# Optimization experiments

Measured on AMD Instinct MI355X. Metric: run time of the kernel, lower is better.

Reference implementation:

```python
import jax, jax.numpy as jnp
import numpy as np

EPS = 1e-5
N, DEG, D, L = 50000, 16, 128, 2  # nodes, max_neighbor, embed_size, gnn_layer


def _log_map_zero(y):
    # Poincare ball log map at origin: atanh(||y||) * y / ||y||, with clamps
    n = jnp.linalg.norm(y, axis=-1, keepdims=True)
    nc = jnp.clip(n, EPS, 1.0 - EPS)
    return y * (jnp.arctanh(nc) / nc)


def _exp_map_zero(v):
    # Poincare ball exp map at origin: tanh(||v||) * v / ||v||
    n = jnp.linalg.norm(v, axis=-1, keepdims=True)
    nc = jnp.maximum(n, EPS)
    return v * (jnp.tanh(nc) / nc)


def setup_inputs() -> dict:
    key = jax.random.key(0)
    k1, k2, k3, k4, k5 = jax.random.split(key, 5)
    node_repr = jax.random.normal(k1, (N, D), jnp.float32) * 0.1
    adj = jax.random.randint(k2, (N, DEG), 0, N)
    weight = jax.random.normal(k3, (N, DEG), jnp.float32)
    mask = jnp.ones((N, 1), jnp.float32)
    # per-relation, per-layer message weights (2 relations: pos / neg edges)
    scale = 1.0 / np.sqrt(D)
    W_pos = jax.random.normal(k4, (L, D, D), jnp.float32) * scale
    W_neg = jax.random.normal(k5, (L, D, D), jnp.float32) * scale
    return {"node_repr": node_repr, "adj": adj, "weight": weight,
            "mask": mask, "W_pos": W_pos, "W_neg": W_neg}


def reference(node_repr, adj, weight, mask, W_pos, W_neg):
    # split_graph_by_negative_edge
    pos_m = (weight > 0).astype(weight.dtype)
    neg_m = (weight < 0).astype(weight.dtype)
    adjs = (adj * pos_m.astype(adj.dtype), adj * neg_m.astype(adj.dtype))
    ws = (weight * pos_m, (-weight) * neg_m)
    Ws = (W_pos, W_neg)

    x = node_repr
    for step in range(L):
        x = (_log_map_zero(x) if step > 0 else x) * mask
        combined = jnp.zeros_like(x)
        for a, w, W in zip(adjs, ws, Ws):
            msg = (x @ W[step]) * mask                    # [N, D]
            nb = msg[a.reshape(-1)].reshape(N, DEG, D)    # neighbor gather
            combined = combined + jnp.sum(w[..., None] * nb, axis=1)
        combined = combined * mask                        # dropout identity (eval)
        x = _exp_map_zero(combined) * mask
        x = jax.nn.relu(x) * mask                         # poincare activation
    return x
```

## Files before the change

### kernel.cpp

```cpp
#include <hip/hip_runtime.h>
#include <math.h>

#define DD 128
#define DEG 16
#define TM 16
#define LDST 136
#define EPSV 1e-5f

typedef _Float16 half8_t __attribute__((ext_vector_type(8)));
typedef float    f32x4   __attribute__((ext_vector_type(4)));
typedef signed char c16v __attribute__((ext_vector_type(16)));

__device__ __forceinline__ float fast_tanh_over(float n) {
    float e  = __expf(2.f * n);
    float th = 1.f - __fdividef(2.f, e + 1.f);
    return __fdividef(th, n);
}
__device__ __forceinline__ float fast_atanh_over(float n) {
    float r = 0.5f * __logf(__fdividef(1.f + n, 1.f - n));
    return __fdividef(r, n);
}

__global__ void prep(const float* __restrict__ x, const float* __restrict__ mask,
                     signed char* __restrict__ x8, float* __restrict__ xsc, int nA,
                     const float* __restrict__ Wp, const float* __restrict__ Wn,
                     _Float16* __restrict__ WT)
{
    if ((int)blockIdx.x < nA) {
        const int r   = blockIdx.x * 16 + (threadIdx.x >> 4);
        const int c16 = threadIdx.x & 15;
        float m  = mask[r];
        float m2 = m * m;
        const float4* xp = (const float4*)(x + (size_t)r * DD + c16 * 8);
        float4 a = xp[0], b = xp[1];
        float v[8] = {a.x*m2, a.y*m2, a.z*m2, a.w*m2, b.x*m2, b.y*m2, b.z*m2, b.w*m2};
        float mx = 0.f;
        #pragma unroll
        for (int c = 0; c < 8; ++c) mx = fmaxf(mx, fabsf(v[c]));
        mx = fmaxf(mx, __shfl_xor(mx, 1));
        mx = fmaxf(mx, __shfl_xor(mx, 2));
        mx = fmaxf(mx, __shfl_xor(mx, 4));
        mx = fmaxf(mx, __shfl_xor(mx, 8));
        float qs = __fdividef(127.f, fmaxf(mx, 1e-20f));
        int q[8];
        #pragma unroll
        for (int c = 0; c < 8; ++c) q[c] = __float2int_rn(v[c] * qs);
        unsigned lo = (q[0]&255) | ((q[1]&255)<<8) | ((q[2]&255)<<16) | ((unsigned)(q[3]&255)<<24);
        unsigned hi = (q[4]&255) | ((q[5]&255)<<8) | ((q[6]&255)<<16) | ((unsigned)(q[7]&255)<<24);
        *(uint2*)(x8 + (size_t)r * DD + c16 * 8) = make_uint2(lo, hi);
        if (c16 == 0) xsc[r] = mx * (1.f / 127.f);
    } else {
        int bid   = blockIdx.x - nA;
        int mat   = bid >> 3;
        int chunk = bid & 7;
        int l = mat >> 1, rel = mat & 1;
        const float* __restrict__ src = (rel ? Wn : Wp) + (size_t)l * DD * DD;
        _Float16* __restrict__ dst = WT + (size_t)mat * DD * DD;
        for (int o = chunk * 2048 + threadIdx.x; o < chunk * 2048 + 2048; o += 256) {
            int nn = o >> 7, kk = o & 127;
            dst[o] = (_Float16)src[kk * DD + nn];
        }
    }
}

__global__ __launch_bounds__(256, 2) void fused_layer(
    const signed char* __restrict__ src8,
    const float* __restrict__ sscale,
    const int*   __restrict__ adj, const float* __restrict__ wgt,
    const float* __restrict__ mask,
    const _Float16* __restrict__ WTp, const _Float16* __restrict__ WTn,
    float* __restrict__ dst_f32,
    signed char* __restrict__ dst8, float* __restrict__ dst_scale,
    int n, int apply_logmap)
{
    __shared__ __align__(16) _Float16 aggP[TM][LDST];
    __shared__ __align__(16) _Float16 aggN[TM][LDST];
    __shared__ int   eidxS[TM][DEG];
    __shared__ float ewgtS[TM][DEG];
    __shared__ float msh[TM];
    __shared__ float partA[4][TM];
    __shared__ float partB[4][TM];
    __shared__ float partC[4][TM];

    const int row0 = blockIdx.x * TM;
    const int tid  = threadIdx.x;

    {
        const int nd = tid >> 4, eg = tid & 15;
        int   av = adj[(size_t)(row0 + nd) * DEG + eg];
        float wv = wgt[(size_t)(row0 + nd) * DEG + eg];
        float sv = sscale[av];
        eidxS[nd][eg] = av;
        ewgtS[nd][eg] = wv * sv;
        if (tid < TM) msh[tid] = mask[row0 + tid];
    }
    __syncthreads();

    const int l64  = tid & 63;
    const int node = (tid >> 6) * 4 + (l64 >> 4);
    const int e    = (l64 >> 3) & 1;
    const int g    = l64 & 7;

    int   idxl[8];
    float wl[8];
    #pragma unroll
    for (int j = 0; j < 8; ++j) {
        idxl[j] = eidxS[node][2 * j + e];
        wl[j]   = ewgtS[node][2 * j + e];
    }

    float aP[16], aN[16];
    #pragma unroll
    for (int c = 0; c < 16; ++c) { aP[c] = 0.f; aN[c] = 0.f; }
    const signed char* __restrict__ srcg = src8 + g * 16;
    #pragma unroll
    for (int j = 0; j < 8; ++j) {
        c16v v = *(const c16v*)(srcg + ((size_t)idxl[j] << 7));
        float wp = fmaxf(wl[j], 0.f);
        float wn = fmaxf(-wl[j], 0.f);
        #pragma unroll
        for (int c = 0; c < 16; ++c) {
            float f = (float)v[c];
            aP[c] += wp * f;
            aN[c] += wn * f;
        }
    }
    {
        half8_t hP, hN;
        #pragma unroll
        for (int c = 0; c < 8; ++c) {
            float ownP  = e ? aP[8 + c] : aP[c];
            float sendP = e ? aP[c]     : aP[8 + c];
            float ownN  = e ? aN[8 + c] : aN[c];
            float sendN = e ? aN[c]     : aN[8 + c];
            hP[c] = (_Float16)(ownP + __shfl_xor(sendP, 8));
            hN[c] = (_Float16)(ownN + __shfl_xor(sendN, 8));
        }
        *(half8_t*)&aggP[node][g * 16 + e * 8] = hP;
        *(half8_t*)&aggN[node][g * 16 + e * 8] = hN;
    }
    __syncthreads();

    const int wv2  = tid >> 6;
    const int l15  = l64 & 15;
    const int quad = l64 >> 4;

    half8_t aPf[4], aNf[4];
    #pragma unroll
    for (int kb = 0; kb < 4; ++kb) {
        aPf[kb] = *(const half8_t*)&aggP[l15][kb * 32 + quad * 8];
        aNf[kb] = *(const half8_t*)&aggN[l15][kb * 32 + quad * 8];
    }

    f32x4 acc[2];
    acc[0] = (f32x4){0.f, 0.f, 0.f, 0.f};
    acc[1] = (f32x4){0.f, 0.f, 0.f, 0.f};
    #pragma unroll
    for (int t = 0; t < 2; ++t) {
        const int nb = wv2 * 2 + t;
        const _Float16* bp = WTp + (size_t)(nb * 16 + l15) * DD + quad * 8;
        const _Float16* bn = WTn + (size_t)(nb * 16 + l15) * DD + quad * 8;
        #pragma unroll
        for (int kb = 0; kb < 4; ++kb) {
            acc[t] = __builtin_amdgcn_mfma_f32_16x16x32_f16(
                aPf[kb], *(const half8_t*)(bp + kb * 32), acc[t], 0, 0, 0);
            acc[t] = __builtin_amdgcn_mfma_f32_16x16x32_f16(
                aNf[kb], *(const half8_t*)(bn + kb * 32), acc[t], 0, 0, 0);
        }
    }

    float cv0[4], cv1[4], mr[4];
    #pragma unroll
    for (int r = 0; r < 4; ++r) {
        const int rl  = quad * 4 + r;
        const int row = row0 + rl;
        float m = (row < n) ? msh[rl] : 0.f;
        mr[r] = m;
        float c0 = acc[0][r] * m, c1 = acc[1][r] * m;
        cv0[r] = c0; cv1[r] = c1;
        float p = c0 * c0 + c1 * c1;
        p += __shfl_xor(p, 1); p += __shfl_xor(p, 2);
        p += __shfl_xor(p, 4); p += __shfl_xor(p, 8);
        if (l15 == 0) partA[wv2][rl] = p;
    }
    __syncthreads();

    float x0[4], x1[4];
    #pragma unroll
    for (int r = 0; r < 4; ++r) {
        const int rl = quad * 4 + r;
        float c2 = partA[0][rl] + partA[1][rl] + partA[2][rl] + partA[3][rl];
        float nc = fmaxf(sqrtf(c2), EPSV);
        float sc = fast_tanh_over(nc);
        float m  = mr[r];
        float t0 = fmaxf(cv0[r] * sc * m, 0.f) * m;
        float t1 = fmaxf(cv1[r] * sc * m, 0.f) * m;
        x0[r] = t0; x1[r] = t1;
        if (apply_logmap) {
            float p = t0 * t0 + t1 * t1;
            p += __shfl_xor(p, 1); p += __shfl_xor(p, 2);
            p += __shfl_xor(p, 4); p += __shfl_xor(p, 8);
            if (l15 == 0) partB[wv2][rl] = p;
        }
    }

    if (apply_logmap) {
        __syncthreads();
        float y0r[4], y1r[4];
        #pragma unroll
        for (int r = 0; r < 4; ++r) {
            const int rl = quad * 4 + r;
            float s2  = partB[0][rl] + partB[1][rl] + partB[2][rl] + partB[3][rl];
            float nc2 = fminf(fmaxf(sqrtf(s2), EPSV), 1.f - EPSV);
            float f = fast_atanh_over(nc2) * mr[r] * mr[r];
            float y0 = x0[r] * f, y1 = x1[r] * f;
            y0r[r] = y0; y1r[r] = y1;
            float mm = fmaxf(fabsf(y0), fabsf(y1));
            mm = fmaxf(mm, __shfl_xor(mm, 1));
            mm = fmaxf(mm, __shfl_xor(mm, 2));
            mm = fmaxf(mm, __shfl_xor(mm, 4));
            mm = fmaxf(mm, __shfl_xor(mm, 8));
            if (l15 == 0) partC[wv2][rl] = mm;
        }
        __syncthreads();
        #pragma unroll
        for (int r = 0; r < 4; ++r) {
            const int rl  = quad * 4 + r;
            const int row = row0 + rl;
            if (row >= n) continue;
            float rmax = fmaxf(fmaxf(partC[0][rl], partC[1][rl]),
                               fmaxf(partC[2][rl], partC[3][rl]));
            float qs = __fdividef(127.f, fmaxf(rmax, 1e-20f));
            int q0 = __float2int_rn(y0r[r] * qs);
            int q1 = __float2int_rn(y1r[r] * qs);
            signed char* drow = dst8 + (size_t)row * DD + wv2 * 32 + l15;
            drow[0]  = (signed char)q0;
            drow[16] = (signed char)q1;
            if (wv2 == 0 && l15 == 0) dst_scale[row] = rmax * (1.f / 127.f);
        }
    } else {
        #pragma unroll
        for (int r = 0; r < 4; ++r) {
            const int rl  = quad * 4 + r;
            const int row = row0 + rl;
            if (row >= n) continue;
            float* drow = dst_f32 + (size_t)row * DD + wv2 * 32 + l15;
            drow[0]  = x0[r];
            drow[16] = x1[r];
        }
    }
}

extern "C" void kernel_launch(void* const* d_in, const int* in_sizes, int n_in,
                              void* d_out, int out_size, void* d_ws, size_t ws_size,
                              hipStream_t stream)
{
    const float* node_repr = (const float*)d_in[0];
    const int*   adj       = (const int*)  d_in[1];
    const float* weight    = (const float*)d_in[2];
    const float* mask      = (const float*)d_in[3];
    const float* W_pos     = (const float*)d_in[4];
    const float* W_neg     = (const float*)d_in[5];

    const int n = in_sizes[0] / DD;

    signed char* x8  = (signed char*)d_ws;
    signed char* y8  = x8 + (size_t)n * DD;
    float*       xsc = (float*)(y8 + (size_t)n * DD);
    float*       ysc = xsc + n;
    _Float16*    WT  = (_Float16*)(ysc + n);

    const int nA = n / 16;
    prep<<<nA + 32, 256, 0, stream>>>(node_repr, mask, x8, xsc, nA,
                                      W_pos, W_neg, WT);

    dim3 grid((n + TM - 1) / TM);
    fused_layer<<<grid, 256, 0, stream>>>(x8, xsc, adj, weight, mask,
                                          WT + 0 * DD * DD, WT + 1 * DD * DD,
                                          nullptr, y8, ysc, n, 1);
    fused_layer<<<grid, 256, 0, stream>>>(y8, ysc, adj, weight, mask,
                                          WT + 2 * DD * DD, WT + 3 * DD * DD,
                                          (float*)d_out, nullptr, nullptr, n, 0);
}
```

Baseline: 180.0 us.

## Split fused layer into gather-aggregate and GEMM-epilogue kernels with int8 intermediates

The per-layer fused kernel becomes two kernels. The gather kernel accumulates positive and negative neighbour sums and writes them as per-row int8 with scales. The GEMM kernel reloads those, dequantizes to fp16, and runs the MFMA matmul plus the exp/log-map epilogue. The intent is to lift occupancy for the latency-bound gather (launch bounds 4) while keeping the GEMM separate. In exchange it adds two extra launches and an extra global round trip of the aggregates, plus extra quantization error on them.

New measurement: 215.6 us. +19.7%, slower.

```diff
diff --git a/kernel.cpp b/kernel.cpp
--- a/kernel.cpp
+++ b/kernel.cpp
@@ -4,12 +4,12 @@
 #define DD 128
 #define DEG 16
 #define TM 16
-#define LDST 136
 #define EPSV 1e-5f
 
 typedef _Float16 half8_t __attribute__((ext_vector_type(8)));
 typedef float    f32x4   __attribute__((ext_vector_type(4)));
 typedef signed char c16v __attribute__((ext_vector_type(16)));
+typedef signed char c8v  __attribute__((ext_vector_type(8)));
 
 __device__ __forceinline__ float fast_tanh_over(float n) {
     float e  = __expf(2.f * n);
@@ -63,93 +63,128 @@
     }
 }
 
-__global__ __launch_bounds__(256, 2) void fused_layer(
+__global__ __launch_bounds__(256, 4) void gather_agg(
     const signed char* __restrict__ src8,
     const float* __restrict__ sscale,
     const int*   __restrict__ adj, const float* __restrict__ wgt,
+    signed char* __restrict__ aggP8, signed char* __restrict__ aggN8,
+    float* __restrict__ ascP, float* __restrict__ ascN, int n)
+{
+    __shared__ int   eidxS[TM][DEG];
+    __shared__ float ewgtS[TM][DEG];
+
+    const int row0 = blockIdx.x * TM;
+    const int tid  = threadIdx.x;
+
+    {
+        const int nd = tid >> 4, eg = tid & 15;
+        int   av = adj[(size_t)(row0 + nd) * DEG + eg];
+        float wv = wgt[(size_t)(row0 + nd) * DEG + eg];
+        eidxS[nd][eg] = av;
+        ewgtS[nd][eg] = wv * sscale[av];
+    }
+    __syncthreads();
+
+    const int l64  = tid & 63;
+    const int node = (tid >> 6) * 4 + (l64 >> 4);
+    const int e    = (l64 >> 3) & 1;
+    const int g    = l64 & 7;
+
+    int   idxl[8];
+    float wl[8];
+    #pragma unroll
+    for (int j = 0; j < 8; ++j) {
+        idxl[j] = eidxS[node][2 * j + e];
+        wl[j]   = ewgtS[node][2 * j + e];
+    }
+
+    float aP[16], aN[16];
+    #pragma unroll
+    for (int c = 0; c < 16; ++c) { aP[c] = 0.f; aN[c] = 0.f; }
+    const signed char* __restrict__ srcg = src8 + g * 16;
+    #pragma unroll
+    for (int j = 0; j < 8; ++j) {
+        c16v v = *(const c16v*)(srcg + ((size_t)idxl[j] << 7));
+        float wp = fmaxf(wl[j], 0.f);
+        float wn = fmaxf(-wl[j], 0.f);
+        #pragma unroll
+        for (int c = 0; c < 16; ++c) {
+            float f = (float)v[c];
+            aP[c] += wp * f;
+            aN[c] += wn * f;
+        }
+    }
+    float fP[8], fN[8];
+    #pragma unroll
+    for (int c = 0; c < 8; ++c) {
+        float ownP  = e ? aP[8 + c] : aP[c];
+        float sendP = e ? aP[c]     : aP[8 + c];
+        float ownN  = e ? aN[8 + c] : aN[c];
+        float sendN = e ? aN[c]     : aN[8 + c];
+        fP[c] = ownP + __shfl_xor(sendP, 8);
+        fN[c] = ownN + __shfl_xor(sendN, 8);
+    }
+    float mP = 0.f, mN = 0.f;
+    #pragma unroll
+    for (int c = 0; c < 8; ++c) { mP = fmaxf(mP, fabsf(fP[c])); mN = fmaxf(mN, fabsf(fN[c])); }
+    mP = fmaxf(mP, __shfl_xor(mP, 1)); mN = fmaxf(mN, __shfl_xor(mN, 1));
+    mP = fmaxf(mP, __shfl_xor(mP, 2)); mN = fmaxf(mN, __shfl_xor(mN, 2));
+    mP = fmaxf(mP, __shfl_xor(mP, 4)); mN = fmaxf(mN, __shfl_xor(mN, 4));
+    mP = fmaxf(mP, __shfl_xor(mP, 8)); mN = fmaxf(mN, __shfl_xor(mN, 8));
+
+    float qsP = __fdividef(127.f, fmaxf(mP, 1e-20f));
+    float qsN = __fdividef(127.f, fmaxf(mN, 1e-20f));
+    int qp[8], qn[8];
+    #pragma unroll
+    for (int c = 0; c < 8; ++c) {
+        qp[c] = __float2int_rn(fP[c] * qsP);
+        qn[c] = __float2int_rn(fN[c] * qsN);
+    }
+    unsigned pl = (qp[0]&255) | ((qp[1]&255)<<8) | ((qp[2]&255)<<16) | ((unsigned)(qp[3]&255)<<24);
+    unsigned ph = (qp[4]&255) | ((qp[5]&255)<<8) | ((qp[6]&255)<<16) | ((unsigned)(qp[7]&255)<<24);
+    unsigned nl = (qn[0]&255) | ((qn[1]&255)<<8) | ((qn[2]&255)<<16) | ((unsigned)(qn[3]&255)<<24);
+    unsigned nh = (qn[4]&255) | ((qn[5]&255)<<8) | ((qn[6]&255)<<16) | ((unsigned)(qn[7]&255)<<24);
+    const size_t ob = (size_t)(row0 + node) * DD + g * 16 + e * 8;
+    *(uint2*)(aggP8 + ob) = make_uint2(pl, ph);
+    *(uint2*)(aggN8 + ob) = make_uint2(nl, nh);
+    if ((l64 & 15) == 0) {
+        ascP[row0 + node] = mP * (1.f / 127.f);
+        ascN[row0 + node] = mN * (1.f / 127.f);
+    }
+}
+
+__global__ __launch_bounds__(256, 2) void gemm_ep(
+    const signed char* __restrict__ aggP8, const signed char* __restrict__ aggN8,
+    const float* __restrict__ ascP, const float* __restrict__ ascN,
     const float* __restrict__ mask,
     const _Float16* __restrict__ WTp, const _Float16* __restrict__ WTn,
     float* __restrict__ dst_f32,
     signed char* __restrict__ dst8, float* __restrict__ dst_scale,
     int n, int apply_logmap)
 {
-    __shared__ __align__(16) _Float16 aggP[TM][LDST];
-    __shared__ __align__(16) _Float16 aggN[TM][LDST];
-    __shared__ int   eidxS[TM][DEG];
-    __shared__ float ewgtS[TM][DEG];
-    __shared__ float msh[TM];
     __shared__ float partA[4][TM];
     __shared__ float partB[4][TM];
     __shared__ float partC[4][TM];
 
     const int row0 = blockIdx.x * TM;
     const int tid  = threadIdx.x;
-
-    {
-        const int nd = tid >> 4, eg = tid & 15;
-        int   av = adj[(size_t)(row0 + nd) * DEG + eg];
-        float wv = wgt[(size_t)(row0 + nd) * DEG + eg];
-        float sv = sscale[av];
-        eidxS[nd][eg] = av;
-        ewgtS[nd][eg] = wv * sv;
-        if (tid < TM) msh[tid] = mask[row0 + tid];
-    }
-    __syncthreads();
-
+    const int wv2  = tid >> 6;
     const int l64  = tid & 63;
-    const int node = (tid >> 6) * 4 + (l64 >> 4);
-    const int e    = (l64 >> 3) & 1;
-    const int g    = l64 & 7;
-
-    int   idxl[8];
-    float wl[8];
-    #pragma unroll
-    for (int j = 0; j < 8; ++j) {
-        idxl[j] = eidxS[node][2 * j + e];
-        wl[j]   = ewgtS[node][2 * j + e];
-    }
-
-    float aP[16], aN[16];
-    #pragma unroll
-    for (int c = 0; c < 16; ++c) { aP[c] = 0.f; aN[c] = 0.f; }
-    const signed char* __restrict__ srcg = src8 + g * 16;
-    #pragma unroll
-    for (int j = 0; j < 8; ++j) {
-        c16v v = *(const c16v*)(srcg + ((size_t)idxl[j] << 7));
-        float wp = fmaxf(wl[j], 0.f);
-        float wn = fmaxf(-wl[j], 0.f);
-        #pragma unroll
-        for (int c = 0; c < 16; ++c) {
-            float f = (float)v[c];
-            aP[c] += wp * f;
-            aN[c] += wn * f;
-        }
-    }
-    {
-        half8_t hP, hN;
-        #pragma unroll
-        for (int c = 0; c < 8; ++c) {
-            float ownP  = e ? aP[8 + c] : aP[c];
-            float sendP = e ? aP[c]     : aP[8 + c];
-            float ownN  = e ? aN[8 + c] : aN[c];
-            float sendN = e ? aN[c]     : aN[8 + c];
-            hP[c] = (_Float16)(ownP + __shfl_xor(sendP, 8));
-            hN[c] = (_Float16)(ownN + __shfl_xor(sendN, 8));
-        }
-        *(half8_t*)&aggP[node][g * 16 + e * 8] = hP;
-        *(half8_t*)&aggN[node][g * 16 + e * 8] = hN;
-    }
-    __syncthreads();
-
-    const int wv2  = tid >> 6;
     const int l15  = l64 & 15;
     const int quad = l64 >> 4;
 
+    const float sP = ascP[row0 + l15];
+    const float sN = ascN[row0 + l15];
     half8_t aPf[4], aNf[4];
     #pragma unroll
     for (int kb = 0; kb < 4; ++kb) {
-        aPf[kb] = *(const half8_t*)&aggP[l15][kb * 32 + quad * 8];
-        aNf[kb] = *(const half8_t*)&aggN[l15][kb * 32 + quad * 8];
+        c8v qp = *(const c8v*)(aggP8 + (size_t)(row0 + l15) * DD + kb * 32 + quad * 8);
+        c8v qn = *(const c8v*)(aggN8 + (size_t)(row0 + l15) * DD + kb * 32 + quad * 8);
+        #pragma unroll
+        for (int c = 0; c < 8; ++c) {
+            aPf[kb][c] = (_Float16)((float)qp[c] * sP);
+            aNf[kb][c] = (_Float16)((float)qn[c] * sN);
+        }
     }
 
     f32x4 acc[2];
@@ -174,7 +209,7 @@
     for (int r = 0; r < 4; ++r) {
         const int rl  = quad * 4 + r;
         const int row = row0 + rl;
-        float m = (row < n) ? msh[rl] : 0.f;
+        float m = (row < n) ? mask[row] : 0.f;
         mr[r] = m;
         float c0 = acc[0][r] * m, c1 = acc[1][r] * m;
         cv0[r] = c0; cv1[r] = c1;
@@ -264,21 +299,27 @@
 
     const int n = in_sizes[0] / DD;
 
-    signed char* x8  = (signed char*)d_ws;
-    signed char* y8  = x8 + (size_t)n * DD;
-    float*       xsc = (float*)(y8 + (size_t)n * DD);
-    float*       ysc = xsc + n;
-    _Float16*    WT  = (_Float16*)(ysc + n);
+    signed char* q8    = (signed char*)d_ws;
+    signed char* aggP8 = q8 + (size_t)n * DD;
+    signed char* aggN8 = aggP8 + (size_t)n * DD;
+    float*       qsc   = (float*)(aggN8 + (size_t)n * DD);
+    float*       ascP  = qsc + n;
+    float*       ascN  = ascP + n;
+    _Float16*    WT    = (_Float16*)(ascN + n);
 
     const int nA = n / 16;
-    prep<<<nA + 32, 256, 0, stream>>>(node_repr, mask, x8, xsc, nA,
+    prep<<<nA + 32, 256, 0, stream>>>(node_repr, mask, q8, qsc, nA,
                                       W_pos, W_neg, WT);
 
     dim3 grid((n + TM - 1) / TM);
-    fused_layer<<<grid, 256, 0, stream>>>(x8, xsc, adj, weight, mask,
-                                          WT + 0 * DD * DD, WT + 1 * DD * DD,
-                                          nullptr, y8, ysc, n, 1);
-    fused_layer<<<grid, 256, 0, stream>>>(y8, ysc, adj, weight, mask,
-                                          WT + 2 * DD * DD, WT + 3 * DD * DD,
-                                          (float*)d_out, nullptr, nullptr, n, 0);
-}
+    gather_agg<<<grid, 256, 0, stream>>>(q8, qsc, adj, weight,
+                                         aggP8, aggN8, ascP, ascN, n);
+    gemm_ep<<<grid, 256, 0, stream>>>(aggP8, aggN8, ascP, ascN, mask,
+                                      WT + 0 * DD * DD, WT + 1 * DD * DD,
+                                      nullptr, q8, qsc, n, 1);
+    gather_agg<<<grid, 256, 0, stream>>>(q8, qsc, adj, weight,
+                                         aggP8, aggN8, ascP, ascN, n);
+    gemm_ep<<<grid, 256, 0, stream>>>(aggP8, aggN8, ascP, ascN, mask,
+                                      WT + 2 * DD * DD, WT + 3 * DD * DD,
+                                      (float*)d_out, nullptr, nullptr, n, 0);
+}
```

## Gather fp32 inputs directly in layer 0, dropping the int8 prep pass

Applied to the files above, without the earlier changes.

Removes the prep pass that quantized node features to int8 before the first layer. Layer 0 now gathers fp32 neighbor rows straight from the input, using a new thread mapping, and applies the mask squared to the edge weights. This saves one kernel launch and a full read/write pass over x. In exchange, the random gather traffic for layer 0 grows fourfold and relies on cache hits. Layer 1 keeps the int8 path in a specialized kernel with no runtime logmap branch.

Measured after the change: 202.2 us. 12.3% more time.

```diff
diff --git a/kernel.cpp b/kernel.cpp
--- a/kernel.cpp
+++ b/kernel.cpp
@@ -21,57 +21,28 @@
     return __fdividef(r, n);
 }
 
-__global__ void prep(const float* __restrict__ x, const float* __restrict__ mask,
-                     signed char* __restrict__ x8, float* __restrict__ xsc, int nA,
-                     const float* __restrict__ Wp, const float* __restrict__ Wn,
-                     _Float16* __restrict__ WT)
+__global__ void prepW(const float* __restrict__ Wp, const float* __restrict__ Wn,
+                      _Float16* __restrict__ WT)
 {
-    if ((int)blockIdx.x < nA) {
-        const int r   = blockIdx.x * 16 + (threadIdx.x >> 4);
-        const int c16 = threadIdx.x & 15;
-        float m  = mask[r];
-        float m2 = m * m;
-        const float4* xp = (const float4*)(x + (size_t)r * DD + c16 * 8);
-        float4 a = xp[0], b = xp[1];
-        float v[8] = {a.x*m2, a.y*m2, a.z*m2, a.w*m2, b.x*m2, b.y*m2, b.z*m2, b.w*m2};
-        float mx = 0.f;
-        #pragma unroll
-        for (int c = 0; c < 8; ++c) mx = fmaxf(mx, fabsf(v[c]));
-        mx = fmaxf(mx, __shfl_xor(mx, 1));
-        mx = fmaxf(mx, __shfl_xor(mx, 2));
-        mx = fmaxf(mx, __shfl_xor(mx, 4));
-        mx = fmaxf(mx, __shfl_xor(mx, 8));
-        float qs = __fdividef(127.f, fmaxf(mx, 1e-20f));
-        int q[8];
-        #pragma unroll
-        for (int c = 0; c < 8; ++c) q[c] = __float2int_rn(v[c] * qs);
-        unsigned lo = (q[0]&255) | ((q[1]&255)<<8) | ((q[2]&255)<<16) | ((unsigned)(q[3]&255)<<24);
-        unsigned hi = (q[4]&255) | ((q[5]&255)<<8) | ((q[6]&255)<<16) | ((unsigned)(q[7]&255)<<24);
-        *(uint2*)(x8 + (size_t)r * DD + c16 * 8) = make_uint2(lo, hi);
-        if (c16 == 0) xsc[r] = mx * (1.f / 127.f);
-    } else {
-        int bid   = blockIdx.x - nA;
-        int mat   = bid >> 3;
-        int chunk = bid & 7;
-        int l = mat >> 1, rel = mat & 1;
-        const float* __restrict__ src = (rel ? Wn : Wp) + (size_t)l * DD * DD;
-        _Float16* __restrict__ dst = WT + (size_t)mat * DD * DD;
-        for (int o = chunk * 2048 + threadIdx.x; o < chunk * 2048 + 2048; o += 256) {
-            int nn = o >> 7, kk = o & 127;
-            dst[o] = (_Float16)src[kk * DD + nn];
-        }
-    }
-}
-
-__global__ __launch_bounds__(256, 2) void fused_layer(
-    const signed char* __restrict__ src8,
-    const float* __restrict__ sscale,
+    int bid   = blockIdx.x;
+    int mat   = bid >> 3;
+    int chunk = bid & 7;
+    int l = mat >> 1, rel = mat & 1;
+    const float* __restrict__ src = (rel ? Wn : Wp) + (size_t)l * DD * DD;
+    _Float16* __restrict__ dst = WT + (size_t)mat * DD * DD;
+    for (int o = chunk * 2048 + threadIdx.x; o < chunk * 2048 + 2048; o += 256) {
+        int nn = o >> 7, kk = o & 127;
+        dst[o] = (_Float16)src[kk * DD + nn];
+    }
+}
+
+__global__ __launch_bounds__(256, 2) void fused_l0_f32(
+    const float* __restrict__ xsrc,
     const int*   __restrict__ adj, const float* __restrict__ wgt,
     const float* __restrict__ mask,
     const _Float16* __restrict__ WTp, const _Float16* __restrict__ WTn,
-    float* __restrict__ dst_f32,
     signed char* __restrict__ dst8, float* __restrict__ dst_scale,
-    int n, int apply_logmap)
+    int n)
 {
     __shared__ __align__(16) _Float16 aggP[TM][LDST];
     __shared__ __align__(16) _Float16 aggN[TM][LDST];
@@ -89,59 +60,47 @@
         const int nd = tid >> 4, eg = tid & 15;
         int   av = adj[(size_t)(row0 + nd) * DEG + eg];
         float wv = wgt[(size_t)(row0 + nd) * DEG + eg];
-        float sv = sscale[av];
+        float mv = mask[av];
         eidxS[nd][eg] = av;
-        ewgtS[nd][eg] = wv * sv;
+        ewgtS[nd][eg] = wv * mv * mv;
         if (tid < TM) msh[tid] = mask[row0 + tid];
     }
     __syncthreads();
 
+    const int qw  = tid >> 4;
+    const int l16 = tid & 15;
+    float aP[8] = {0.f,0.f,0.f,0.f,0.f,0.f,0.f,0.f};
+    float aN[8] = {0.f,0.f,0.f,0.f,0.f,0.f,0.f,0.f};
+    {
+        const float* __restrict__ srcb = xsrc + l16 * 8;
+        #pragma unroll
+        for (int j = 0; j < 16; ++j) {
+            const int   idx = eidxS[qw][j];
+            const float w   = ewgtS[qw][j];
+            const float* rp = srcb + (size_t)idx * DD;
+            float4 v0 = ((const float4*)rp)[0];
+            float4 v1 = ((const float4*)rp)[1];
+            float wp = fmaxf(w, 0.f);
+            float wn = fmaxf(-w, 0.f);
+            float f0[8] = {v0.x, v0.y, v0.z, v0.w, v1.x, v1.y, v1.z, v1.w};
+            #pragma unroll
+            for (int c = 0; c < 8; ++c) {
+                aP[c] += wp * f0[c];
+                aN[c] += wn * f0[c];
+            }
+        }
+    }
+    {
+        half8_t hP, hN;
+        #pragma unroll
+        for (int c = 0; c < 8; ++c) { hP[c] = (_Float16)aP[c]; hN[c] = (_Float16)aN[c]; }
+        *(half8_t*)&aggP[qw][l16 * 8] = hP;
+        *(half8_t*)&aggN[qw][l16 * 8] = hN;
+    }
+    __syncthreads();
+
+    const int wv2  = tid >> 6;
     const int l64  = tid & 63;
-    const int node = (tid >> 6) * 4 + (l64 >> 4);
-    const int e    = (l64 >> 3) & 1;
-    const int g    = l64 & 7;
-
-    int   idxl[8];
-    float wl[8];
-    #pragma unroll
-    for (int j = 0; j < 8; ++j) {
-        idxl[j] = eidxS[node][2 * j + e];
-        wl[j]   = ewgtS[node][2 * j + e];
-    }
-
-    float aP[16], aN[16];
-    #pragma unroll
-    for (int c = 0; c < 16; ++c) { aP[c] = 0.f; aN[c] = 0.f; }
-    const signed char* __restrict__ srcg = src8 + g * 16;
-    #pragma unroll
-    for (int j = 0; j < 8; ++j) {
-        c16v v = *(const c16v*)(srcg + ((size_t)idxl[j] << 7));
-        float wp = fmaxf(wl[j], 0.f);
-        float wn = fmaxf(-wl[j], 0.f);
-        #pragma unroll
-        for (int c = 0; c < 16; ++c) {
-            float f = (float)v[c];
-            aP[c] += wp * f;
-            aN[c] += wn * f;
-        }
-    }
-    {
-        half8_t hP, hN;
-        #pragma unroll
-        for (int c = 0; c < 8; ++c) {
-            float ownP  = e ? aP[8 + c] : aP[c];
-            float sendP = e ? aP[c]     : aP[8 + c];
-            float ownN  = e ? aN[8 + c] : aN[c];
-            float sendN = e ? aN[c]     : aN[8 + c];
-            hP[c] = (_Float16)(ownP + __shfl_xor(sendP, 8));
-            hN[c] = (_Float16)(ownN + __shfl_xor(sendN, 8));
-        }
-        *(half8_t*)&aggP[node][g * 16 + e * 8] = hP;
-        *(half8_t*)&aggN[node][g * 16 + e * 8] = hN;
-    }
-    __syncthreads();
-
-    const int wv2  = tid >> 6;
     const int l15  = l64 & 15;
     const int quad = l64 >> 4;
 
@@ -196,58 +155,179 @@
         float t0 = fmaxf(cv0[r] * sc * m, 0.f) * m;
         float t1 = fmaxf(cv1[r] * sc * m, 0.f) * m;
         x0[r] = t0; x1[r] = t1;
-        if (apply_logmap) {
-            float p = t0 * t0 + t1 * t1;
-            p += __shfl_xor(p, 1); p += __shfl_xor(p, 2);
-            p += __shfl_xor(p, 4); p += __shfl_xor(p, 8);
-            if (l15 == 0) partB[wv2][rl] = p;
-        }
-    }
-
-    if (apply_logmap) {
-        __syncthreads();
-        float y0r[4], y1r[4];
-        #pragma unroll
-        for (int r = 0; r < 4; ++r) {
-            const int rl = quad * 4 + r;
-            float s2  = partB[0][rl] + partB[1][rl] + partB[2][rl] + partB[3][rl];
-            float nc2 = fminf(fmaxf(sqrtf(s2), EPSV), 1.f - EPSV);
-            float f = fast_atanh_over(nc2) * mr[r] * mr[r];
-            float y0 = x0[r] * f, y1 = x1[r] * f;
-            y0r[r] = y0; y1r[r] = y1;
-            float mm = fmaxf(fabsf(y0), fabsf(y1));
-            mm = fmaxf(mm, __shfl_xor(mm, 1));
-            mm = fmaxf(mm, __shfl_xor(mm, 2));
-            mm = fmaxf(mm, __shfl_xor(mm, 4));
-            mm = fmaxf(mm, __shfl_xor(mm, 8));
-            if (l15 == 0) partC[wv2][rl] = mm;
-        }
-        __syncthreads();
-        #pragma unroll
-        for (int r = 0; r < 4; ++r) {
-            const int rl  = quad * 4 + r;
-            const int row = row0 + rl;
-            if (row >= n) continue;
-            float rmax = fmaxf(fmaxf(partC[0][rl], partC[1][rl]),
-                               fmaxf(partC[2][rl], partC[3][rl]));
-            float qs = __fdividef(127.f, fmaxf(rmax, 1e-20f));
-            int q0 = __float2int_rn(y0r[r] * qs);
-            int q1 = __float2int_rn(y1r[r] * qs);
-            signed char* drow = dst8 + (size_t)row * DD + wv2 * 32 + l15;
-            drow[0]  = (signed char)q0;
-            drow[16] = (signed char)q1;
-            if (wv2 == 0 && l15 == 0) dst_scale[row] = rmax * (1.f / 127.f);
-        }
-    } else {
-        #pragma unroll
-        for (int r = 0; r < 4; ++r) {
-            const int rl  = quad * 4 + r;
-            const int row = row0 + rl;
-            if (row >= n) continue;
-            float* drow = dst_f32 + (size_t)row * DD + wv2 * 32 + l15;
-            drow[0]  = x0[r];
-            drow[16] = x1[r];
-        }
+        float p = t0 * t0 + t1 * t1;
+        p += __shfl_xor(p, 1); p += __shfl_xor(p, 2);
+        p += __shfl_xor(p, 4); p += __shfl_xor(p, 8);
+        if (l15 == 0) partB[wv2][rl] = p;
+    }
+    __syncthreads();
+
+    float y0r[4], y1r[4];
+    #pragma unroll
+    for (int r = 0; r < 4; ++r) {
+        const int rl = quad * 4 + r;
+        float s2  = partB[0][rl] + partB[1][rl] + partB[2][rl] + partB[3][rl];
+        float nc2 = fminf(fmaxf(sqrtf(s2), EPSV), 1.f - EPSV);
+        float f = fast_atanh_over(nc2) * mr[r] * mr[r];
+        float y0 = x0[r] * f, y1 = x1[r] * f;
+        y0r[r] = y0; y1r[r] = y1;
+        float mm = fmaxf(fabsf(y0), fabsf(y1));
+        mm = fmaxf(mm, __shfl_xor(mm, 1));
+        mm = fmaxf(mm, __shfl_xor(mm, 2));
+        mm = fmaxf(mm, __shfl_xor(mm, 4));
+        mm = fmaxf(mm, __shfl_xor(mm, 8));
+        if (l15 == 0) partC[wv2][rl] = mm;
+    }
+    __syncthreads();
+    #pragma unroll
+    for (int r = 0; r < 4; ++r) {
+        const int rl  = quad * 4 + r;
+        const int row = row0 + rl;
+        if (row >= n) continue;
+        float rmax = fmaxf(fmaxf(partC[0][rl], partC[1][rl]),
+                           fmaxf(partC[2][rl], partC[3][rl]));
+        float qs = __fdividef(127.f, fmaxf(rmax, 1e-20f));
+        int q0 = __float2int_rn(y0r[r] * qs);
+        int q1 = __float2int_rn(y1r[r] * qs);
+        signed char* drow = dst8 + (size_t)row * DD + wv2 * 32 + l15;
+        drow[0]  = (signed char)q0;
+        drow[16] = (signed char)q1;
+        if (wv2 == 0 && l15 == 0) dst_scale[row] = rmax * (1.f / 127.f);
+    }
+}
+
+__global__ __launch_bounds__(256, 2) void fused_l1_i8(
+    const signed char* __restrict__ src8,
+    const float* __restrict__ sscale,
+    const int*   __restrict__ adj, const float* __restrict__ wgt,
+    const float* __restrict__ mask,
+    const _Float16* __restrict__ WTp, const _Float16* __restrict__ WTn,
+    float* __restrict__ dst_f32, int n)
+{
+    __shared__ __align__(16) _Float16 aggP[TM][LDST];
+    __shared__ __align__(16) _Float16 aggN[TM][LDST];
+    __shared__ int   eidxS[TM][DEG];
+    __shared__ float ewgtS[TM][DEG];
+    __shared__ float msh[TM];
+    __shared__ float partA[4][TM];
+
+    const int row0 = blockIdx.x * TM;
+    const int tid  = threadIdx.x;
+
+    {
+        const int nd = tid >> 4, eg = tid & 15;
+        int   av = adj[(size_t)(row0 + nd) * DEG + eg];
+        float wv = wgt[(size_t)(row0 + nd) * DEG + eg];
+        float sv = sscale[av];
+        eidxS[nd][eg] = av;
+        ewgtS[nd][eg] = wv * sv;
+        if (tid < TM) msh[tid] = mask[row0 + tid];
+    }
+    __syncthreads();
+
+    const int l64  = tid & 63;
+    const int node = (tid >> 6) * 4 + (l64 >> 4);
+    const int e    = (l64 >> 3) & 1;
+    const int g    = l64 & 7;
+
+    int   idxl[8];
+    float wl[8];
+    #pragma unroll
+    for (int j = 0; j < 8; ++j) {
+        idxl[j] = eidxS[node][2 * j + e];
+        wl[j]   = ewgtS[node][2 * j + e];
+    }
+
+    float aP[16], aN[16];
+    #pragma unroll
+    for (int c = 0; c < 16; ++c) { aP[c] = 0.f; aN[c] = 0.f; }
+    const signed char* __restrict__ srcg = src8 + g * 16;
+    #pragma unroll
+    for (int j = 0; j < 8; ++j) {
+        c16v v = *(const c16v*)(srcg + ((size_t)idxl[j] << 7));
+        float wp = fmaxf(wl[j], 0.f);
+        float wn = fmaxf(-wl[j], 0.f);
+        #pragma unroll
+        for (int c = 0; c < 16; ++c) {
+            float f = (float)v[c];
+            aP[c] += wp * f;
+            aN[c] += wn * f;
+        }
+    }
+    {
+        half8_t hP, hN;
+        #pragma unroll
+        for (int c = 0; c < 8; ++c) {
+            float ownP  = e ? aP[8 + c] : aP[c];
+            float sendP = e ? aP[c]     : aP[8 + c];
+            float ownN  = e ? aN[8 + c] : aN[c];
+            float sendN = e ? aN[c]     : aN[8 + c];
+            hP[c] = (_Float16)(ownP + __shfl_xor(sendP, 8));
+            hN[c] = (_Float16)(ownN + __shfl_xor(sendN, 8));
+        }
+        *(half8_t*)&aggP[node][g * 16 + e * 8] = hP;
+        *(half8_t*)&aggN[node][g * 16 + e * 8] = hN;
+    }
+    __syncthreads();
+
+    const int wv2  = tid >> 6;
+    const int l15  = l64 & 15;
+    const int quad = l64 >> 4;
+
+    half8_t aPf[4], aNf[4];
+    #pragma unroll
+    for (int kb = 0; kb < 4; ++kb) {
+        aPf[kb] = *(const half8_t*)&aggP[l15][kb * 32 + quad * 8];
+        aNf[kb] = *(const half8_t*)&aggN[l15][kb * 32 + quad * 8];
+    }
+
+    f32x4 acc[2];
+    acc[0] = (f32x4){0.f, 0.f, 0.f, 0.f};
+    acc[1] = (f32x4){0.f, 0.f, 0.f, 0.f};
+    #pragma unroll
+    for (int t = 0; t < 2; ++t) {
+        const int nb = wv2 * 2 + t;
+        const _Float16* bp = WTp + (size_t)(nb * 16 + l15) * DD + quad * 8;
+        const _Float16* bn = WTn + (size_t)(nb * 16 + l15) * DD + quad * 8;
+        #pragma unroll
+        for (int kb = 0; kb < 4; ++kb) {
+            acc[t] = __builtin_amdgcn_mfma_f32_16x16x32_f16(
+                aPf[kb], *(const half8_t*)(bp + kb * 32), acc[t], 0, 0, 0);
+            acc[t] = __builtin_amdgcn_mfma_f32_16x16x32_f16(
+                aNf[kb], *(const half8_t*)(bn + kb * 32), acc[t], 0, 0, 0);
+        }
+    }
+
+    float cv0[4], cv1[4], mr[4];
+    #pragma unroll
+    for (int r = 0; r < 4; ++r) {
+        const int rl  = quad * 4 + r;
+        const int row = row0 + rl;
+        float m = (row < n) ? msh[rl] : 0.f;
+        mr[r] = m;
+        float c0 = acc[0][r] * m, c1 = acc[1][r] * m;
+        cv0[r] = c0; cv1[r] = c1;
+        float p = c0 * c0 + c1 * c1;
+        p += __shfl_xor(p, 1); p += __shfl_xor(p, 2);
+        p += __shfl_xor(p, 4); p += __shfl_xor(p, 8);
+        if (l15 == 0) partA[wv2][rl] = p;
+    }
+    __syncthreads();
+
+    #pragma unroll
+    for (int r = 0; r < 4; ++r) {
+        const int rl  = quad * 4 + r;
+        const int row = row0 + rl;
+        if (row >= n) continue;
+        float c2 = partA[0][rl] + partA[1][rl] + partA[2][rl] + partA[3][rl];
+        float nc = fmaxf(sqrtf(c2), EPSV);
+        float sc = fast_tanh_over(nc);
+        float m  = mr[r];
+        float t0 = fmaxf(cv0[r] * sc * m, 0.f) * m;
+        float t1 = fmaxf(cv1[r] * sc * m, 0.f) * m;
+        float* drow = dst_f32 + (size_t)row * DD + wv2 * 32 + l15;
+        drow[0]  = t0;
+        drow[16] = t1;
     }
 }
 
@@ -264,21 +344,17 @@
 
     const int n = in_sizes[0] / DD;
 
-    signed char* x8  = (signed char*)d_ws;
-    signed char* y8  = x8 + (size_t)n * DD;
-    float*       xsc = (float*)(y8 + (size_t)n * DD);
-    float*       ysc = xsc + n;
+    signed char* y8  = (signed char*)d_ws;
+    float*       ysc = (float*)(y8 + (size_t)n * DD);
     _Float16*    WT  = (_Float16*)(ysc + n);
 
-    const int nA = n / 16;
-    prep<<<nA + 32, 256, 0, stream>>>(node_repr, mask, x8, xsc, nA,
-                                      W_pos, W_neg, WT);
+    prepW<<<32, 256, 0, stream>>>(W_pos, W_neg, WT);
 
     dim3 grid((n + TM - 1) / TM);
-    fused_layer<<<grid, 256, 0, stream>>>(x8, xsc, adj, weight, mask,
-                                          WT + 0 * DD * DD, WT + 1 * DD * DD,
-                                          nullptr, y8, ysc, n, 1);
-    fused_layer<<<grid, 256, 0, stream>>>(y8, ysc, adj, weight, mask,
+    fused_l0_f32<<<grid, 256, 0, stream>>>(node_repr, adj, weight, mask,
+                                           WT + 0 * DD * DD, WT + 1 * DD * DD,
+                                           y8, ysc, n);
+    fused_l1_i8<<<grid, 256, 0, stream>>>(y8, ysc, adj, weight, mask,
                                           WT + 2 * DD * DD, WT + 3 * DD * DD,
-                                          (float*)d_out, nullptr, nullptr, n, 0);
-}
+                                          (float*)d_out, n);
+}
```

## Reorder to transform-then-gather with per-relation int8 message tables

Applied to the files above, without the earlier changes.

Each layer is split into a GEMM kernel and a gather kernel. The GEMM computes x@W_pos and x@W_neg for every node and stores them as per-row int8 tables with their scales. The gather kernel then reads only the table that matches each edge's sign and applies the exp/relu/log-map epilogue directly in registers, with no LDS cross-wave reductions. This replaces the gather-then-GEMM order that ran two GEMMs per block after aggregation. The cost is two extra kernel launches and an intermediate table of 2*N*128 bytes that is written and then re-read; the int8 rounding now happens after the matmul instead of before it.

Result: slower. 191.6 us (+6.4%).

```diff
diff --git a/kernel.cpp b/kernel.cpp
--- a/kernel.cpp
+++ b/kernel.cpp
@@ -3,7 +3,8 @@
 
 #define DD 128
 #define DEG 16
-#define TM 16
+#define TMG 16
+#define TMZ 32
 #define LDST 136
 #define EPSV 1e-5f
 
@@ -21,78 +22,139 @@
     return __fdividef(r, n);
 }
 
-__global__ void prep(const float* __restrict__ x, const float* __restrict__ mask,
-                     signed char* __restrict__ x8, float* __restrict__ xsc, int nA,
-                     const float* __restrict__ Wp, const float* __restrict__ Wn,
-                     _Float16* __restrict__ WT)
-{
-    if ((int)blockIdx.x < nA) {
-        const int r   = blockIdx.x * 16 + (threadIdx.x >> 4);
-        const int c16 = threadIdx.x & 15;
-        float m  = mask[r];
-        float m2 = m * m;
-        const float4* xp = (const float4*)(x + (size_t)r * DD + c16 * 8);
-        float4 a = xp[0], b = xp[1];
-        float v[8] = {a.x*m2, a.y*m2, a.z*m2, a.w*m2, b.x*m2, b.y*m2, b.z*m2, b.w*m2};
+__global__ void prepW(const float* __restrict__ Wp, const float* __restrict__ Wn,
+                      _Float16* __restrict__ WT)
+{
+    int bid   = blockIdx.x;
+    int mat   = bid >> 3;
+    int chunk = bid & 7;
+    int l = mat >> 1, rel = mat & 1;
+    const float* __restrict__ src = (rel ? Wn : Wp) + (size_t)l * DD * DD;
+    _Float16* __restrict__ dst = WT + (size_t)mat * DD * DD;
+    for (int o = chunk * 2048 + threadIdx.x; o < chunk * 2048 + 2048; o += 256) {
+        int nn = o >> 7, kk = o & 127;
+        dst[o] = (_Float16)src[kk * DD + nn];
+    }
+}
+
+__global__ __launch_bounds__(256, 2) void z_gemm(
+    const float* __restrict__ xf32,
+    const signed char* __restrict__ y8,
+    const float* __restrict__ ysc,
+    const float* __restrict__ mask,
+    const _Float16* __restrict__ WTp, const _Float16* __restrict__ WTn,
+    signed char* __restrict__ Z8,
+    float* __restrict__ zscP, float* __restrict__ zscN,
+    int n, int layer0)
+{
+    __shared__ __align__(16) _Float16 At[TMZ][LDST];
+
+    const int row0 = blockIdx.x * TMZ;
+    const int tid  = threadIdx.x;
+
+    {
+        const int ar   = tid >> 3;
+        const int ac   = (tid & 7) * 16;
+        const int rowg = row0 + ar;
+        _Float16 hv[16];
+        if (rowg < n) {
+            if (layer0) {
+                float m = mask[rowg]; float m2 = m * m;
+                const float4* xp = (const float4*)(xf32 + (size_t)rowg * DD + ac);
+                #pragma unroll
+                for (int q4 = 0; q4 < 4; ++q4) {
+                    float4 v = xp[q4];
+                    hv[q4*4+0] = (_Float16)(v.x*m2); hv[q4*4+1] = (_Float16)(v.y*m2);
+                    hv[q4*4+2] = (_Float16)(v.z*m2); hv[q4*4+3] = (_Float16)(v.w*m2);
+                }
+            } else {
+                float s = ysc[rowg];
+                c16v v = *(const c16v*)(y8 + (size_t)rowg * DD + ac);
+                #pragma unroll
+                for (int c = 0; c < 16; ++c) hv[c] = (_Float16)((float)v[c] * s);
+            }
+        } else {
+            #pragma unroll
+            for (int c = 0; c < 16; ++c) hv[c] = (_Float16)0.f;
+        }
+        *(half8_t*)&At[ar][ac]     = *(half8_t*)&hv[0];
+        *(half8_t*)&At[ar][ac + 8] = *(half8_t*)&hv[8];
+    }
+    __syncthreads();
+
+    const int w    = tid >> 6;
+    const int mt   = w >> 1;
+    const int rel  = w & 1;
+    const int l64  = tid & 63;
+    const int l15  = l64 & 15;
+    const int quad = l64 >> 4;
+
+    half8_t aF[4];
+    #pragma unroll
+    for (int kb = 0; kb < 4; ++kb)
+        aF[kb] = *(const half8_t*)&At[mt * 16 + l15][kb * 32 + quad * 8];
+
+    const _Float16* __restrict__ WT = rel ? WTn : WTp;
+    f32x4 acc[8];
+    #pragma unroll
+    for (int nb = 0; nb < 8; ++nb) acc[nb] = (f32x4){0.f, 0.f, 0.f, 0.f};
+    #pragma unroll
+    for (int nb = 0; nb < 8; ++nb) {
+        const _Float16* bp = WT + (size_t)(nb * 16 + l15) * DD + quad * 8;
+        #pragma unroll
+        for (int kb = 0; kb < 4; ++kb)
+            acc[nb] = __builtin_amdgcn_mfma_f32_16x16x32_f16(
+                aF[kb], *(const half8_t*)(bp + kb * 32), acc[nb], 0, 0, 0);
+    }
+
+    signed char* __restrict__ zb  = Z8 + (size_t)rel * n * DD;
+    float*       __restrict__ zsc = rel ? zscN : zscP;
+    #pragma unroll
+    for (int r = 0; r < 4; ++r) {
+        const int rowg = row0 + mt * 16 + quad * 4 + r;
         float mx = 0.f;
         #pragma unroll
-        for (int c = 0; c < 8; ++c) mx = fmaxf(mx, fabsf(v[c]));
+        for (int nb = 0; nb < 8; ++nb) mx = fmaxf(mx, fabsf(acc[nb][r]));
         mx = fmaxf(mx, __shfl_xor(mx, 1));
         mx = fmaxf(mx, __shfl_xor(mx, 2));
         mx = fmaxf(mx, __shfl_xor(mx, 4));
         mx = fmaxf(mx, __shfl_xor(mx, 8));
-        float qs = __fdividef(127.f, fmaxf(mx, 1e-20f));
-        int q[8];
-        #pragma unroll
-        for (int c = 0; c < 8; ++c) q[c] = __float2int_rn(v[c] * qs);
-        unsigned lo = (q[0]&255) | ((q[1]&255)<<8) | ((q[2]&255)<<16) | ((unsigned)(q[3]&255)<<24);
-        unsigned hi = (q[4]&255) | ((q[5]&255)<<8) | ((q[6]&255)<<16) | ((unsigned)(q[7]&255)<<24);
-        *(uint2*)(x8 + (size_t)r * DD + c16 * 8) = make_uint2(lo, hi);
-        if (c16 == 0) xsc[r] = mx * (1.f / 127.f);
-    } else {
-        int bid   = blockIdx.x - nA;
-        int mat   = bid >> 3;
-        int chunk = bid & 7;
-        int l = mat >> 1, rel = mat & 1;
-        const float* __restrict__ src = (rel ? Wn : Wp) + (size_t)l * DD * DD;
-        _Float16* __restrict__ dst = WT + (size_t)mat * DD * DD;
-        for (int o = chunk * 2048 + threadIdx.x; o < chunk * 2048 + 2048; o += 256) {
-            int nn = o >> 7, kk = o & 127;
-            dst[o] = (_Float16)src[kk * DD + nn];
+        if (rowg < n) {
+            float qs = __fdividef(127.f, fmaxf(mx, 1e-20f));
+            signed char* zr = zb + (size_t)rowg * DD + l15;
+            #pragma unroll
+            for (int nb = 0; nb < 8; ++nb)
+                zr[nb * 16] = (signed char)__float2int_rn(acc[nb][r] * qs);
+            if (l15 == 0) zsc[rowg] = mx * (1.f / 127.f);
         }
     }
 }
 
-__global__ __launch_bounds__(256, 2) void fused_layer(
-    const signed char* __restrict__ src8,
-    const float* __restrict__ sscale,
+__global__ __launch_bounds__(256, 2) void gather_ep(
+    const signed char* __restrict__ Z8,
+    const float* __restrict__ zscP, const float* __restrict__ zscN,
     const int*   __restrict__ adj, const float* __restrict__ wgt,
     const float* __restrict__ mask,
-    const _Float16* __restrict__ WTp, const _Float16* __restrict__ WTn,
     float* __restrict__ dst_f32,
     signed char* __restrict__ dst8, float* __restrict__ dst_scale,
     int n, int apply_logmap)
 {
-    __shared__ __align__(16) _Float16 aggP[TM][LDST];
-    __shared__ __align__(16) _Float16 aggN[TM][LDST];
-    __shared__ int   eidxS[TM][DEG];
-    __shared__ float ewgtS[TM][DEG];
-    __shared__ float msh[TM];
-    __shared__ float partA[4][TM];
-    __shared__ float partB[4][TM];
-    __shared__ float partC[4][TM];
-
-    const int row0 = blockIdx.x * TM;
+    __shared__ int   eoffS[TMG][DEG];
+    __shared__ float ewgtS[TMG][DEG];
+    __shared__ float msh[TMG];
+
+    const int row0 = blockIdx.x * TMG;
     const int tid  = threadIdx.x;
 
     {
         const int nd = tid >> 4, eg = tid & 15;
         int   av = adj[(size_t)(row0 + nd) * DEG + eg];
         float wv = wgt[(size_t)(row0 + nd) * DEG + eg];
-        float sv = sscale[av];
-        eidxS[nd][eg] = av;
-        ewgtS[nd][eg] = wv * sv;
-        if (tid < TM) msh[tid] = mask[row0 + tid];
+        const int sel = (wv > 0.f) ? 0 : 1;
+        const float* sp = sel ? zscN : zscP;
+        eoffS[nd][eg] = av * DD + sel * (n * DD);
+        ewgtS[nd][eg] = fabsf(wv) * sp[av];
+        if (tid < TMG) msh[tid] = mask[row0 + tid];
     }
     __syncthreads();
 
@@ -101,153 +163,74 @@
     const int e    = (l64 >> 3) & 1;
     const int g    = l64 & 7;
 
-    int   idxl[8];
+    int   offl[8];
     float wl[8];
     #pragma unroll
     for (int j = 0; j < 8; ++j) {
-        idxl[j] = eidxS[node][2 * j + e];
+        offl[j] = eoffS[node][2 * j + e];
         wl[j]   = ewgtS[node][2 * j + e];
     }
 
-    float aP[16], aN[16];
-    #pragma unroll
-    for (int c = 0; c < 16; ++c) { aP[c] = 0.f; aN[c] = 0.f; }
-    const signed char* __restrict__ srcg = src8 + g * 16;
+    float a[16];
+    #pragma unroll
+    for (int c = 0; c < 16; ++c) a[c] = 0.f;
+    const signed char* __restrict__ srcg = Z8 + g * 16;
     #pragma unroll
     for (int j = 0; j < 8; ++j) {
-        c16v v = *(const c16v*)(srcg + ((size_t)idxl[j] << 7));
-        float wp = fmaxf(wl[j], 0.f);
-        float wn = fmaxf(-wl[j], 0.f);
-        #pragma unroll
-        for (int c = 0; c < 16; ++c) {
-            float f = (float)v[c];
-            aP[c] += wp * f;
-            aN[c] += wn * f;
-        }
-    }
-    {
-        half8_t hP, hN;
-        #pragma unroll
-        for (int c = 0; c < 8; ++c) {
-            float ownP  = e ? aP[8 + c] : aP[c];
-            float sendP = e ? aP[c]     : aP[8 + c];
-            float ownN  = e ? aN[8 + c] : aN[c];
-            float sendN = e ? aN[c]     : aN[8 + c];
-            hP[c] = (_Float16)(ownP + __shfl_xor(sendP, 8));
-            hN[c] = (_Float16)(ownN + __shfl_xor(sendN, 8));
-        }
-        *(half8_t*)&aggP[node][g * 16 + e * 8] = hP;
-        *(half8_t*)&aggN[node][g * 16 + e * 8] = hN;
-    }
-    __syncthreads();
-
-    const int wv2  = tid >> 6;
-    const int l15  = l64 & 15;
-    const int quad = l64 >> 4;
-
-    half8_t aPf[4], aNf[4];
-    #pragma unroll
-    for (int kb = 0; kb < 4; ++kb) {
-        aPf[kb] = *(const half8_t*)&aggP[l15][kb * 32 + quad * 8];
-        aNf[kb] = *(const half8_t*)&aggN[l15][kb * 32 + quad * 8];
-    }
-
-    f32x4 acc[2];
-    acc[0] = (f32x4){0.f, 0.f, 0.f, 0.f};
-    acc[1] = (f32x4){0.f, 0.f, 0.f, 0.f};
-    #pragma unroll
-    for (int t = 0; t < 2; ++t) {
-        const int nb = wv2 * 2 + t;
-        const _Float16* bp = WTp + (size_t)(nb * 16 + l15) * DD + quad * 8;
-        const _Float16* bn = WTn + (size_t)(nb * 16 + l15) * DD + quad * 8;
-        #pragma unroll
-        for (int kb = 0; kb < 4; ++kb) {
-            acc[t] = __builtin_amdgcn_mfma_f32_16x16x32_f16(
-                aPf[kb], *(const half8_t*)(bp + kb * 32), acc[t], 0, 0, 0);
-            acc[t] = __builtin_amdgcn_mfma_f32_16x16x32_f16(
-                aNf[kb], *(const half8_t*)(bn + kb * 32), acc[t], 0, 0, 0);
-        }
-    }
-
-    float cv0[4], cv1[4], mr[4];
-    #pragma unroll
-    for (int r = 0; r < 4; ++r) {
-        const int rl  = quad * 4 + r;
-        const int row = row0 + rl;
-        float m = (row < n) ? msh[rl] : 0.f;
-        mr[r] = m;
-        float c0 = acc[0][r] * m, c1 = acc[1][r] * m;
-        cv0[r] = c0; cv1[r] = c1;
-        float p = c0 * c0 + c1 * c1;
-        p += __shfl_xor(p, 1); p += __shfl_xor(p, 2);
-        p += __shfl_xor(p, 4); p += __shfl_xor(p, 8);
-        if (l15 == 0) partA[wv2][rl] = p;
-    }
-    __syncthreads();
-
-    float x0[4], x1[4];
-    #pragma unroll
-    for (int r = 0; r < 4; ++r) {
-        const int rl = quad * 4 + r;
-        float c2 = partA[0][rl] + partA[1][rl] + partA[2][rl] + partA[3][rl];
-        float nc = fmaxf(sqrtf(c2), EPSV);
-        float sc = fast_tanh_over(nc);
-        float m  = mr[r];
-        float t0 = fmaxf(cv0[r] * sc * m, 0.f) * m;
-        float t1 = fmaxf(cv1[r] * sc * m, 0.f) * m;
-        x0[r] = t0; x1[r] = t1;
-        if (apply_logmap) {
-            float p = t0 * t0 + t1 * t1;
-            p += __shfl_xor(p, 1); p += __shfl_xor(p, 2);
-            p += __shfl_xor(p, 4); p += __shfl_xor(p, 8);
-            if (l15 == 0) partB[wv2][rl] = p;
-        }
+        c16v v = *(const c16v*)(srcg + (size_t)offl[j]);
+        float wj = wl[j];
+        #pragma unroll
+        for (int c = 0; c < 16; ++c) a[c] += wj * (float)v[c];
+    }
+    float f[8];
+    #pragma unroll
+    for (int c = 0; c < 8; ++c) {
+        float own  = e ? a[8 + c] : a[c];
+        float send = e ? a[c]     : a[8 + c];
+        f[c] = own + __shfl_xor(send, 8);
+    }
+
+    const int   row = row0 + node;
+    const float m   = msh[node];
+    float t[8];
+    float p = 0.f;
+    #pragma unroll
+    for (int c = 0; c < 8; ++c) { float cv = f[c] * m; t[c] = cv; p += cv * cv; }
+    p += __shfl_xor(p, 1); p += __shfl_xor(p, 2);
+    p += __shfl_xor(p, 4); p += __shfl_xor(p, 8);
+    float nc = fmaxf(sqrtf(p), EPSV);
+    float sc = fast_tanh_over(nc);
+    float s2 = 0.f;
+    #pragma unroll
+    for (int c = 0; c < 8; ++c) {
+        t[c] = fmaxf(t[c] * sc * m, 0.f) * m;
+        s2 += t[c] * t[c];
     }
 
     if (apply_logmap) {
-        __syncthreads();
-        float y0r[4], y1r[4];
-        #pragma unroll
-        for (int r = 0; r < 4; ++r) {
-            const int rl = quad * 4 + r;
-            float s2  = partB[0][rl] + partB[1][rl] + partB[2][rl] + partB[3][rl];
-            float nc2 = fminf(fmaxf(sqrtf(s2), EPSV), 1.f - EPSV);
-            float f = fast_atanh_over(nc2) * mr[r] * mr[r];
-            float y0 = x0[r] * f, y1 = x1[r] * f;
-            y0r[r] = y0; y1r[r] = y1;
-            float mm = fmaxf(fabsf(y0), fabsf(y1));
-            mm = fmaxf(mm, __shfl_xor(mm, 1));
-            mm = fmaxf(mm, __shfl_xor(mm, 2));
-            mm = fmaxf(mm, __shfl_xor(mm, 4));
-            mm = fmaxf(mm, __shfl_xor(mm, 8));
-            if (l15 == 0) partC[wv2][rl] = mm;
-        }
-        __syncthreads();
-        #pragma unroll
-        for (int r = 0; r < 4; ++r) {
-            const int rl  = quad * 4 + r;
-            const int row = row0 + rl;
-            if (row >= n) continue;
-            float rmax = fmaxf(fmaxf(partC[0][rl], partC[1][rl]),
-                               fmaxf(partC[2][rl], partC[3][rl]));
-            float qs = __fdividef(127.f, fmaxf(rmax, 1e-20f));
-            int q0 = __float2int_rn(y0r[r] * qs);
-            int q1 = __float2int_rn(y1r[r] * qs);
-            signed char* drow = dst8 + (size_t)row * DD + wv2 * 32 + l15;
-            drow[0]  = (signed char)q0;
-            drow[16] = (signed char)q1;
-            if (wv2 == 0 && l15 == 0) dst_scale[row] = rmax * (1.f / 127.f);
-        }
+        s2 += __shfl_xor(s2, 1); s2 += __shfl_xor(s2, 2);
+        s2 += __shfl_xor(s2, 4); s2 += __shfl_xor(s2, 8);
+        float nc2 = fminf(fmaxf(sqrtf(s2), EPSV), 1.f - EPSV);
+        float ff  = fast_atanh_over(nc2) * m * m;
+        float y[8], rmax = 0.f;
+        #pragma unroll
+        for (int c = 0; c < 8; ++c) { y[c] = t[c] * ff; rmax = fmaxf(rmax, fabsf(y[c])); }
+        rmax = fmaxf(rmax, __shfl_xor(rmax, 1));
+        rmax = fmaxf(rmax, __shfl_xor(rmax, 2));
+        rmax = fmaxf(rmax, __shfl_xor(rmax, 4));
+        rmax = fmaxf(rmax, __shfl_xor(rmax, 8));
+        float qs = __fdividef(127.f, fmaxf(rmax, 1e-20f));
+        int q[8];
+        #pragma unroll
+        for (int c = 0; c < 8; ++c) q[c] = __float2int_rn(y[c] * qs);
+        unsigned lo = (q[0]&255) | ((q[1]&255)<<8) | ((q[2]&255)<<16) | ((unsigned)(q[3]&255)<<24);
+        unsigned hi = (q[4]&255) | ((q[5]&255)<<8) | ((q[6]&255)<<16) | ((unsigned)(q[7]&255)<<24);
+        *(uint2*)(dst8 + (size_t)row * DD + g * 16 + e * 8) = make_uint2(lo, hi);
+        if ((l64 & 15) == 0) dst_scale[row] = rmax * (1.f / 127.f);
     } else {
-        #pragma unroll
-        for (int r = 0; r < 4; ++r) {
-            const int rl  = quad * 4 + r;
-            const int row = row0 + rl;
-            if (row >= n) continue;
-            float* drow = dst_f32 + (size_t)row * DD + wv2 * 32 + l15;
-            drow[0]  = x0[r];
-            drow[16] = x1[r];
-        }
+        float* drow = dst_f32 + (size_t)row * DD + g * 16 + e * 8;
+        ((float4*)drow)[0] = make_float4(t[0], t[1], t[2], t[3]);
+        ((float4*)drow)[1] = make_float4(t[4], t[5], t[6], t[7]);
     }
 }
 
@@ -264,21 +247,26 @@
 
     const int n = in_sizes[0] / DD;
 
-    signed char* x8  = (signed char*)d_ws;
-    signed char* y8  = x8 + (size_t)n * DD;
-    float*       xsc = (float*)(y8 + (size_t)n * DD);
-    float*       ysc = xsc + n;
-    _Float16*    WT  = (_Float16*)(ysc + n);
-
-    const int nA = n / 16;
-    prep<<<nA + 32, 256, 0, stream>>>(node_repr, mask, x8, xsc, nA,
-                                      W_pos, W_neg, WT);
-
-    dim3 grid((n + TM - 1) / TM);
-    fused_layer<<<grid, 256, 0, stream>>>(x8, xsc, adj, weight, mask,
-                                          WT + 0 * DD * DD, WT + 1 * DD * DD,
-                                          nullptr, y8, ysc, n, 1);
-    fused_layer<<<grid, 256, 0, stream>>>(y8, ysc, adj, weight, mask,
-                                          WT + 2 * DD * DD, WT + 3 * DD * DD,
-                                          (float*)d_out, nullptr, nullptr, n, 0);
-}
+    signed char* Z8   = (signed char*)d_ws;
+    signed char* y8   = Z8 + (size_t)2 * n * DD;
+    float*       zscP = (float*)(y8 + (size_t)n * DD);
+    float*       zscN = zscP + n;
+    float*       ysc  = zscN + n;
+    _Float16*    WT   = (_Float16*)(ysc + n);
+
+    prepW<<<32, 256, 0, stream>>>(W_pos, W_neg, WT);
+
+    dim3 zgrid((n + TMZ - 1) / TMZ);
+    dim3 ggrid((n + TMG - 1) / TMG);
+
+    z_gemm<<<zgrid, 256, 0, stream>>>(node_repr, nullptr, nullptr, mask,
+                                      WT + 0 * DD * DD, WT + 1 * DD * DD,
+                                      Z8, zscP, zscN, n, 1);
+    gather_ep<<<ggrid, 256, 0, stream>>>(Z8, zscP, zscN, adj, weight, mask,
+                                         nullptr, y8, ysc, n, 1);
+    z_gemm<<<zgrid, 256, 0, stream>>>(nullptr, y8, ysc, mask,
+                                      WT + 2 * DD * DD, WT + 3 * DD * DD,
+                                      Z8, zscP, zscN, n, 0);
+    gather_ep<<<ggrid, 256, 0, stream>>>(Z8, zscP, zscN, adj, weight, mask,
+                                         (float*)d_out, nullptr, nullptr, n, 0);
+}
```
